# Optimization experiments

Measured on AMD Instinct MI355X. Metric: run time of the kernel, lower is better.

Reference implementation:

```python
import jax, jax.numpy as jnp
import numpy as np


def setup_inputs() -> dict:
    key = jax.random.key(0)
    k1, k2, k3 = jax.random.split(key, 3)
    B, L, d = 4, 9, 256
    n_nodes = (B ** L - 1) // (B - 1)  # complete B-ary tree, level order
    vectors = jax.random.normal(k1, (n_nodes, d), dtype=jnp.float32)
    scale = 1.0 / np.sqrt(d)
    Wl = jax.random.normal(k2, (d, d), dtype=jnp.float32) * scale
    Wr = jax.random.normal(k3, (d, d), dtype=jnp.float32) * scale
    return {"vectors": vectors, "Wl": Wl, "Wr": Wr, "branching": B, "n_levels": L}


def reference(vectors, Wl, Wr, branching, n_levels):
    # Complete branching-ary tree stored in level (BFS) order.
    # Leaf: h = vector. Internal: h = tanh(sum_i lc_i*Wl@h_i + rc_i*Wr@h_i + vector)
    B = int(branching)
    L = int(n_levels)
    sizes = [B ** l for l in range(L)]
    offsets = np.concatenate([[0], np.cumsum(sizes)])
    ind = jnp.arange(1, B + 1, dtype=vectors.dtype)
    if B > 1:
        lc = (B - ind) / (B - 1)   # [B]
        rc = (ind - 1) / (B - 1)
    else:
        lc = jnp.full((B,), 0.5, dtype=vectors.dtype)
        rc = jnp.full((B,), 0.5, dtype=vectors.dtype)
    # leaves
    h = vectors[offsets[L - 1]:offsets[L]]  # [B^(L-1), d]
    for l in range(L - 2, -1, -1):
        n_par = sizes[l]
        hl = (h @ Wl.T).reshape(n_par, B, -1)  # [n_par, B, d]
        hr = (h @ Wr.T).reshape(n_par, B, -1)
        contrib = (lc[None, :, None] * hl + rc[None, :, None] * hr).sum(axis=1)
        h = jnp.tanh(contrib + vectors[offsets[l]:offsets[l + 1]])
    return h  # root state, [1, d]
```

## Files before the change

kernel.cpp:

```cpp
#include <hip/hip_runtime.h>
#include <math.h>


typedef __bf16 bf16x8 __attribute__((ext_vector_type(8)));
typedef __bf16 bf16x4 __attribute__((ext_vector_type(4)));
typedef float f32x4 __attribute__((ext_vector_type(4)));

__device__ __forceinline__ float fast_tanh(float x) {
    float ax = fabsf(x);
    float t = __builtin_amdgcn_exp2f(ax * -2.885390082f);
    float r = (1.0f - t) * __builtin_amdgcn_rcpf(1.0f + t);
    return copysignf(r, x);
}

__global__ __launch_bounds__(256) void cbt_wconv(
    const float* __restrict__ Wl, const float* __restrict__ Wr,
    __bf16* __restrict__ Wfrag)
{
    const int t = blockIdx.x * 256 + threadIdx.x;
    const int L = t & 63;
    const int TJ = t >> 6;
    const int T = TJ & 15;
    const int J = TJ >> 4;
    const int n = J * 16 + (L & 15);
    const int k = T * 32 + (L >> 4) * 8;
    const float* src = (k < 256) ? (Wl + (size_t)n * 256 + k)
                                 : (Wr + (size_t)n * 256 + (k - 256));
    const float4 f0 = *reinterpret_cast<const float4*>(src);
    const float4 f1 = *reinterpret_cast<const float4*>(src + 4);
    bf16x8 o;
    o[0] = (__bf16)f0.x; o[1] = (__bf16)f0.y; o[2] = (__bf16)f0.z; o[3] = (__bf16)f0.w;
    o[4] = (__bf16)f1.x; o[5] = (__bf16)f1.y; o[6] = (__bf16)f1.z; o[7] = (__bf16)f1.w;
    *reinterpret_cast<bf16x8*>(Wfrag + (size_t)t * 8) = o;
}

template <typename CT, typename OT>
__global__ __launch_bounds__(256, 2) void cbt_mfma(
    const CT* __restrict__ h,
    const __bf16* __restrict__ Wfrag,
    const float* __restrict__ vec,
    OT* __restrict__ out)
{
    __shared__ __align__(16) __bf16 Alds[4 * 32 * 40];

    const int tid = threadIdx.x;
    const int lane = tid & 63;
    const int w = tid >> 6;
    const int wr = w >> 1, wc = w & 1;
    const int mBase = blockIdx.x * 32;

    f32x4 acc[8] = {};

    const int sm  = tid >> 3;
    const int skq = (tid & 7) * 4;
    const CT* hb = h + (size_t)(mBase + sm) * 1024 + skq;

    float c0[4], c1[4], c2[4], c3[4];
    auto load_h = [&](int k0) {
        if constexpr (sizeof(CT) == 4) {
            const float4 a = *reinterpret_cast<const float4*>(hb + k0);
            const float4 b = *reinterpret_cast<const float4*>(hb + k0 + 256);
            const float4 c = *reinterpret_cast<const float4*>(hb + k0 + 512);
            const float4 d = *reinterpret_cast<const float4*>(hb + k0 + 768);
            c0[0] = a.x; c0[1] = a.y; c0[2] = a.z; c0[3] = a.w;
            c1[0] = b.x; c1[1] = b.y; c1[2] = b.z; c1[3] = b.w;
            c2[0] = c.x; c2[1] = c.y; c2[2] = c.z; c2[3] = c.w;
            c3[0] = d.x; c3[1] = d.y; c3[2] = d.z; c3[3] = d.w;
        } else {
            const bf16x4 a = *reinterpret_cast<const bf16x4*>(hb + k0);
            const bf16x4 b = *reinterpret_cast<const bf16x4*>(hb + k0 + 256);
            const bf16x4 c = *reinterpret_cast<const bf16x4*>(hb + k0 + 512);
            const bf16x4 d = *reinterpret_cast<const bf16x4*>(hb + k0 + 768);
#pragma unroll
            for (int j = 0; j < 4; ++j) {
                c0[j] = (float)a[j]; c1[j] = (float)b[j];
                c2[j] = (float)c[j]; c3[j] = (float)d[j];
            }
        }
    };

    auto store_A = [&]() {
        constexpr float C23 = 2.0f / 3.0f, C13 = 1.0f / 3.0f;
        bf16x4 glh, gll, grh, grl;
#pragma unroll
        for (int j = 0; j < 4; ++j) {
            const float gl = c0[j] + C23 * c1[j] + C13 * c2[j];
            const float gr = C13 * c1[j] + C23 * c2[j] + c3[j];
            glh[j] = (__bf16)gl;
            gll[j] = (__bf16)(gl - (float)glh[j]);
            grh[j] = (__bf16)gr;
            grl[j] = (__bf16)(gr - (float)grh[j]);
        }
        const int o = sm * 40 + skq;
        *reinterpret_cast<bf16x4*>(&Alds[o])        = glh;
        *reinterpret_cast<bf16x4*>(&Alds[o + 1280]) = gll;
        *reinterpret_cast<bf16x4*>(&Alds[o + 2560]) = grh;
        *reinterpret_cast<bf16x4*>(&Alds[o + 3840]) = grl;
    };

    bf16x8 bfr[2][8];
    const __bf16* Wb = Wfrag + ((size_t)wc * 128 * 64 + lane) * 8;
    auto load_B = [&](int s, int buf) {
        const __bf16* p = Wb + (size_t)s * 512;
#pragma unroll
        for (int j = 0; j < 8; ++j)
            bfr[buf][j] = *reinterpret_cast<const bf16x8*>(p + (size_t)j * 8192);
    };

    load_h(0);
    load_B(0, 0);
    load_B(8, 1);

    const int arow = (wr * 16 + (lane & 15)) * 40 + (lane >> 4) * 8;

    for (int T = 0; T < 8; ++T) {
        __syncthreads();
        store_A();
        __syncthreads();

        if (T < 7) load_h((T + 1) * 32);

        const bf16x8 afLh = *reinterpret_cast<const bf16x8*>(&Alds[arow]);
        const bf16x8 afLl = *reinterpret_cast<const bf16x8*>(&Alds[arow + 1280]);
#pragma unroll
        for (int j = 0; j < 8; ++j)
            acc[j] = __builtin_amdgcn_mfma_f32_16x16x32_bf16(
                afLh, bfr[0][j], acc[j], 0, 0, 0);
#pragma unroll
        for (int j = 0; j < 8; ++j)
            acc[j] = __builtin_amdgcn_mfma_f32_16x16x32_bf16(
                afLl, bfr[0][j], acc[j], 0, 0, 0);

        if (T < 7) load_B(T + 1, 0);

        const bf16x8 afRh = *reinterpret_cast<const bf16x8*>(&Alds[arow + 2560]);
        const bf16x8 afRl = *reinterpret_cast<const bf16x8*>(&Alds[arow + 3840]);
#pragma unroll
        for (int j = 0; j < 8; ++j)
            acc[j] = __builtin_amdgcn_mfma_f32_16x16x32_bf16(
                afRh, bfr[1][j], acc[j], 0, 0, 0);
#pragma unroll
        for (int j = 0; j < 8; ++j)
            acc[j] = __builtin_amdgcn_mfma_f32_16x16x32_bf16(
                afRl, bfr[1][j], acc[j], 0, 0, 0);

        if (T < 7) load_B(T + 9, 1);
    }

    const int q = lane >> 4, n16 = lane & 15;
    const int mrow = mBase + wr * 16 + q * 4;
#pragma unroll
    for (int j = 0; j < 8; ++j) {
        const int n = wc * 128 + j * 16 + n16;
#pragma unroll
        for (int r = 0; r < 4; ++r) {
            const size_t idx = (size_t)(mrow + r) * 256 + n;
            out[idx] = (OT)fast_tanh(acc[j][r] + vec[idx]);
        }
    }
}

__global__ __launch_bounds__(256) void cbt_small(
    const float* __restrict__ h, const float* __restrict__ Wl,
    const float* __restrict__ Wr, const float* __restrict__ vec,
    float* __restrict__ out)
{
    const int w = blockIdx.x * 4 + (threadIdx.x >> 6);
    const int lane = threadIdx.x & 63;
    const int m = w >> 8;
    const int n = w & 255;

    const float* hbp = h + (size_t)m * 1024 + lane * 4;
    const float4 c0 = *reinterpret_cast<const float4*>(hbp);
    const float4 c1 = *reinterpret_cast<const float4*>(hbp + 256);
    const float4 c2 = *reinterpret_cast<const float4*>(hbp + 512);
    const float4 c3 = *reinterpret_cast<const float4*>(hbp + 768);
    const float4 wl = *reinterpret_cast<const float4*>(Wl + (size_t)n * 256 + lane * 4);
    const float4 wr = *reinterpret_cast<const float4*>(Wr + (size_t)n * 256 + lane * 4);

    constexpr float C23 = 2.0f / 3.0f;
    constexpr float C13 = 1.0f / 3.0f;
    const float f0[4] = {c0.x, c0.y, c0.z, c0.w};
    const float f1[4] = {c1.x, c1.y, c1.z, c1.w};
    const float f2[4] = {c2.x, c2.y, c2.z, c2.w};
    const float f3[4] = {c3.x, c3.y, c3.z, c3.w};
    const float wlv[4] = {wl.x, wl.y, wl.z, wl.w};
    const float wrv[4] = {wr.x, wr.y, wr.z, wr.w};
    float acc = 0.0f;
#pragma unroll
    for (int j = 0; j < 4; ++j) {
        const float gl = f0[j] + C23 * f1[j] + C13 * f2[j];
        const float gr = C13 * f1[j] + C23 * f2[j] + f3[j];
        acc += gl * wlv[j] + gr * wrv[j];
    }
#pragma unroll
    for (int off = 32; off >= 1; off >>= 1) acc += __shfl_xor(acc, off, 64);

    if (lane == 0)
        out[(size_t)m * 256 + n] = fast_tanh(acc + vec[(size_t)m * 256 + n]);
}

extern "C" void kernel_launch(void* const* d_in, const int* in_sizes, int n_in,
                              void* d_out, int out_size, void* d_ws, size_t ws_size,
                              hipStream_t stream) {
    const float* vectors = (const float*)d_in[0];
    const float* Wl = (const float*)d_in[1];
    const float* Wr = (const float*)d_in[2];

    char* p = (char*)d_ws;
    __bf16* buf7 = (__bf16*)p;           p += (size_t)16384 * 256 * 2;
    float*  buf6 = (float*)p;            p += (size_t)4096 * 256 * 4;
    float*  buf5 = (float*)p;            p += (size_t)1024 * 256 * 4;
    float*  buf4 = (float*)p;            p += (size_t)256 * 256 * 4;
    float*  buf3 = (float*)p;            p += (size_t)64 * 256 * 4;
    float*  buf2 = (float*)p;            p += (size_t)16 * 256 * 4;
    float*  buf1 = (float*)p;            p += (size_t)4 * 256 * 4;
    __bf16* Wfrag = (__bf16*)p;

    size_t offsets[10];
    offsets[0] = 0;
    size_t sz = 1;
    for (int l = 0; l < 9; ++l) { offsets[l + 1] = offsets[l] + sz; sz *= 4; }

    hipLaunchKernelGGL(cbt_wconv, dim3(64), dim3(256), 0, stream, Wl, Wr, Wfrag);

    const float* leaf = vectors + offsets[8] * 256;

    hipLaunchKernelGGL((cbt_mfma<float, __bf16>), dim3(512), dim3(256), 0, stream,
                       leaf, Wfrag, vectors + offsets[7] * 256, buf7);
    hipLaunchKernelGGL((cbt_mfma<__bf16, float>), dim3(128), dim3(256), 0, stream,
                       buf7, Wfrag, vectors + offsets[6] * 256, buf6);
    hipLaunchKernelGGL((cbt_mfma<float, float>), dim3(32), dim3(256), 0, stream,
                       buf6, Wfrag, vectors + offsets[5] * 256, buf5);
    hipLaunchKernelGGL((cbt_mfma<float, float>), dim3(8), dim3(256), 0, stream,
                       buf5, Wfrag, vectors + offsets[4] * 256, buf4);
    hipLaunchKernelGGL(cbt_small, dim3(64 * 64), dim3(256), 0, stream,
                       buf4, Wl, Wr, vectors + offsets[3] * 256, buf3);
    hipLaunchKernelGGL(cbt_small, dim3(16 * 64), dim3(256), 0, stream,
                       buf3, Wl, Wr, vectors + offsets[2] * 256, buf2);
    hipLaunchKernelGGL(cbt_small, dim3(4 * 64), dim3(256), 0, stream,
                       buf2, Wl, Wr, vectors + offsets[1] * 256, buf1);
    hipLaunchKernelGGL(cbt_small, dim3(1 * 64), dim3(256), 0, stream,
                       buf1, Wl, Wr, vectors + offsets[0] * 256, (float*)d_out);
}
```

Measured before the change: 190.0 us.

## Fuse all tree levels into one cooperative persistent kernel with grid syncs

Replaces the nine separate kernel launches (weight conversion, four MFMA levels, four small levels) with a single cooperative kernel. Grid-wide syncs separate the levels, and grid-stride loops let each block handle several tiles or outputs. The aim is to remove per-launch overhead and inter-kernel gaps, which dominate the tiny upper levels. In exchange it adds grid.sync cost at each level, and the grid is capped at 512 blocks with hardcoded offsets.

```diff
diff --git a/kernel.cpp b/kernel.cpp
--- a/kernel.cpp
+++ b/kernel.cpp
@@ -1,5 +1,8 @@
 #include <hip/hip_runtime.h>
+#include <hip/hip_cooperative_groups.h>
 #include <math.h>
+
+namespace cg = cooperative_groups;
 
 
 typedef __bf16 bf16x8 __attribute__((ext_vector_type(8)));
@@ -13,41 +16,41 @@
     return copysignf(r, x);
 }
 
-__global__ __launch_bounds__(256) void cbt_wconv(
+__device__ __forceinline__ void wconv_body(
     const float* __restrict__ Wl, const float* __restrict__ Wr,
     __bf16* __restrict__ Wfrag)
 {
-    const int t = blockIdx.x * 256 + threadIdx.x;
-    const int L = t & 63;
-    const int TJ = t >> 6;
-    const int T = TJ & 15;
-    const int J = TJ >> 4;
-    const int n = J * 16 + (L & 15);
-    const int k = T * 32 + (L >> 4) * 8;
-    const float* src = (k < 256) ? (Wl + (size_t)n * 256 + k)
-                                 : (Wr + (size_t)n * 256 + (k - 256));
-    const float4 f0 = *reinterpret_cast<const float4*>(src);
-    const float4 f1 = *reinterpret_cast<const float4*>(src + 4);
-    bf16x8 o;
-    o[0] = (__bf16)f0.x; o[1] = (__bf16)f0.y; o[2] = (__bf16)f0.z; o[3] = (__bf16)f0.w;
-    o[4] = (__bf16)f1.x; o[5] = (__bf16)f1.y; o[6] = (__bf16)f1.z; o[7] = (__bf16)f1.w;
-    *reinterpret_cast<bf16x8*>(Wfrag + (size_t)t * 8) = o;
+    for (int t = blockIdx.x * 256 + (int)threadIdx.x; t < 16384;
+         t += gridDim.x * 256) {
+        const int L = t & 63;
+        const int TJ = t >> 6;
+        const int T = TJ & 15;
+        const int J = TJ >> 4;
+        const int n = J * 16 + (L & 15);
+        const int k = T * 32 + (L >> 4) * 8;
+        const float* src = (k < 256) ? (Wl + (size_t)n * 256 + k)
+                                     : (Wr + (size_t)n * 256 + (k - 256));
+        const float4 f0 = *reinterpret_cast<const float4*>(src);
+        const float4 f1 = *reinterpret_cast<const float4*>(src + 4);
+        bf16x8 o;
+        o[0] = (__bf16)f0.x; o[1] = (__bf16)f0.y; o[2] = (__bf16)f0.z; o[3] = (__bf16)f0.w;
+        o[4] = (__bf16)f1.x; o[5] = (__bf16)f1.y; o[6] = (__bf16)f1.z; o[7] = (__bf16)f1.w;
+        *reinterpret_cast<bf16x8*>(Wfrag + (size_t)t * 8) = o;
+    }
 }
 
 template <typename CT, typename OT>
-__global__ __launch_bounds__(256, 2) void cbt_mfma(
+__device__ __forceinline__ void mfma_body(
     const CT* __restrict__ h,
     const __bf16* __restrict__ Wfrag,
     const float* __restrict__ vec,
-    OT* __restrict__ out)
-{
-    __shared__ __align__(16) __bf16 Alds[4 * 32 * 40];
-
+    OT* __restrict__ out,
+    int mBase, __bf16* Alds)
+{
     const int tid = threadIdx.x;
     const int lane = tid & 63;
     const int w = tid >> 6;
     const int wr = w >> 1, wc = w & 1;
-    const int mBase = blockIdx.x * 32;
 
     f32x4 acc[8] = {};
 
@@ -160,44 +163,93 @@
     }
 }
 
-__global__ __launch_bounds__(256) void cbt_small(
+__device__ __forceinline__ void small_body(
     const float* __restrict__ h, const float* __restrict__ Wl,
     const float* __restrict__ Wr, const float* __restrict__ vec,
-    float* __restrict__ out)
-{
-    const int w = blockIdx.x * 4 + (threadIdx.x >> 6);
+    float* __restrict__ out, int nout)
+{
+    const int gw = blockIdx.x * 4 + ((int)threadIdx.x >> 6);
     const int lane = threadIdx.x & 63;
-    const int m = w >> 8;
-    const int n = w & 255;
-
-    const float* hbp = h + (size_t)m * 1024 + lane * 4;
-    const float4 c0 = *reinterpret_cast<const float4*>(hbp);
-    const float4 c1 = *reinterpret_cast<const float4*>(hbp + 256);
-    const float4 c2 = *reinterpret_cast<const float4*>(hbp + 512);
-    const float4 c3 = *reinterpret_cast<const float4*>(hbp + 768);
-    const float4 wl = *reinterpret_cast<const float4*>(Wl + (size_t)n * 256 + lane * 4);
-    const float4 wr = *reinterpret_cast<const float4*>(Wr + (size_t)n * 256 + lane * 4);
-
-    constexpr float C23 = 2.0f / 3.0f;
-    constexpr float C13 = 1.0f / 3.0f;
-    const float f0[4] = {c0.x, c0.y, c0.z, c0.w};
-    const float f1[4] = {c1.x, c1.y, c1.z, c1.w};
-    const float f2[4] = {c2.x, c2.y, c2.z, c2.w};
-    const float f3[4] = {c3.x, c3.y, c3.z, c3.w};
-    const float wlv[4] = {wl.x, wl.y, wl.z, wl.w};
-    const float wrv[4] = {wr.x, wr.y, wr.z, wr.w};
-    float acc = 0.0f;
-#pragma unroll
-    for (int j = 0; j < 4; ++j) {
-        const float gl = f0[j] + C23 * f1[j] + C13 * f2[j];
-        const float gr = C13 * f1[j] + C23 * f2[j] + f3[j];
-        acc += gl * wlv[j] + gr * wrv[j];
-    }
-#pragma unroll
-    for (int off = 32; off >= 1; off >>= 1) acc += __shfl_xor(acc, off, 64);
-
-    if (lane == 0)
-        out[(size_t)m * 256 + n] = fast_tanh(acc + vec[(size_t)m * 256 + n]);
+    const int nw = gridDim.x * 4;
+
+    for (int o = gw; o < nout; o += nw) {
+        const int m = o >> 8;
+        const int n = o & 255;
+
+        const float* hbp = h + (size_t)m * 1024 + lane * 4;
+        const float4 c0 = *reinterpret_cast<const float4*>(hbp);
+        const float4 c1 = *reinterpret_cast<const float4*>(hbp + 256);
+        const float4 c2 = *reinterpret_cast<const float4*>(hbp + 512);
+        const float4 c3 = *reinterpret_cast<const float4*>(hbp + 768);
+        const float4 wl = *reinterpret_cast<const float4*>(Wl + (size_t)n * 256 + lane * 4);
+        const float4 wr = *reinterpret_cast<const float4*>(Wr + (size_t)n * 256 + lane * 4);
+
+        constexpr float C23 = 2.0f / 3.0f;
+        constexpr float C13 = 1.0f / 3.0f;
+        const float f0[4] = {c0.x, c0.y, c0.z, c0.w};
+        const float f1[4] = {c1.x, c1.y, c1.z, c1.w};
+        const float f2[4] = {c2.x, c2.y, c2.z, c2.w};
+        const float f3[4] = {c3.x, c3.y, c3.z, c3.w};
+        const float wlv[4] = {wl.x, wl.y, wl.z, wl.w};
+        const float wrv[4] = {wr.x, wr.y, wr.z, wr.w};
+        float acc = 0.0f;
+#pragma unroll
+        for (int j = 0; j < 4; ++j) {
+            const float gl = f0[j] + C23 * f1[j] + C13 * f2[j];
+            const float gr = C13 * f1[j] + C23 * f2[j] + f3[j];
+            acc += gl * wlv[j] + gr * wrv[j];
+        }
+#pragma unroll
+        for (int off = 32; off >= 1; off >>= 1) acc += __shfl_xor(acc, off, 64);
+
+        if (lane == 0)
+            out[(size_t)m * 256 + n] = fast_tanh(acc + vec[(size_t)m * 256 + n]);
+    }
+}
+
+__global__ __launch_bounds__(256, 2) void cbt_all(
+    const float* __restrict__ vectors,
+    const float* __restrict__ Wl, const float* __restrict__ Wr,
+    float* __restrict__ outF,
+    __bf16* __restrict__ buf7, float* __restrict__ buf6,
+    float* __restrict__ buf5, float* __restrict__ buf4,
+    float* __restrict__ buf3, float* __restrict__ buf2,
+    float* __restrict__ buf1, __bf16* __restrict__ Wfrag)
+{
+    __shared__ __align__(16) __bf16 Alds[4 * 32 * 40];
+
+    cg::grid_group grid = cg::this_grid();
+
+    wconv_body(Wl, Wr, Wfrag);
+    grid.sync();
+
+    for (int t = blockIdx.x; t < 512; t += gridDim.x)
+        mfma_body<float, __bf16>(vectors + (size_t)21845 * 256, Wfrag,
+                                 vectors + (size_t)5461 * 256, buf7, t * 32, Alds);
+    grid.sync();
+
+    for (int t = blockIdx.x; t < 128; t += gridDim.x)
+        mfma_body<__bf16, float>(buf7, Wfrag,
+                                 vectors + (size_t)1365 * 256, buf6, t * 32, Alds);
+    grid.sync();
+
+    for (int t = blockIdx.x; t < 32; t += gridDim.x)
+        mfma_body<float, float>(buf6, Wfrag,
+                                vectors + (size_t)341 * 256, buf5, t * 32, Alds);
+    grid.sync();
+
+    for (int t = blockIdx.x; t < 8; t += gridDim.x)
+        mfma_body<float, float>(buf5, Wfrag,
+                                vectors + (size_t)85 * 256, buf4, t * 32, Alds);
+    grid.sync();
+
+    small_body(buf4, Wl, Wr, vectors + (size_t)21 * 256, buf3, 64 * 256);
+    grid.sync();
+    small_body(buf3, Wl, Wr, vectors + (size_t)5 * 256, buf2, 16 * 256);
+    grid.sync();
+    small_body(buf2, Wl, Wr, vectors + (size_t)1 * 256, buf1, 4 * 256);
+    grid.sync();
+    small_body(buf1, Wl, Wr, vectors, outF, 1 * 256);
 }
 
 extern "C" void kernel_launch(void* const* d_in, const int* in_sizes, int n_in,
@@ -206,6 +258,7 @@
     const float* vectors = (const float*)d_in[0];
     const float* Wl = (const float*)d_in[1];
     const float* Wr = (const float*)d_in[2];
+    float* outF = (float*)d_out;
 
     char* p = (char*)d_ws;
     __bf16* buf7 = (__bf16*)p;           p += (size_t)16384 * 256 * 2;
@@ -217,29 +270,18 @@
     float*  buf1 = (float*)p;            p += (size_t)4 * 256 * 4;
     __bf16* Wfrag = (__bf16*)p;
 
-    size_t offsets[10];
-    offsets[0] = 0;
-    size_t sz = 1;
-    for (int l = 0; l < 9; ++l) { offsets[l + 1] = offsets[l] + sz; sz *= 4; }
-
-    hipLaunchKernelGGL(cbt_wconv, dim3(64), dim3(256), 0, stream, Wl, Wr, Wfrag);
-
-    const float* leaf = vectors + offsets[8] * 256;
-
-    hipLaunchKernelGGL((cbt_mfma<float, __bf16>), dim3(512), dim3(256), 0, stream,
-                       leaf, Wfrag, vectors + offsets[7] * 256, buf7);
-    hipLaunchKernelGGL((cbt_mfma<__bf16, float>), dim3(128), dim3(256), 0, stream,
-                       buf7, Wfrag, vectors + offsets[6] * 256, buf6);
-    hipLaunchKernelGGL((cbt_mfma<float, float>), dim3(32), dim3(256), 0, stream,
-                       buf6, Wfrag, vectors + offsets[5] * 256, buf5);
-    hipLaunchKernelGGL((cbt_mfma<float, float>), dim3(8), dim3(256), 0, stream,
-                       buf5, Wfrag, vectors + offsets[4] * 256, buf4);
-    hipLaunchKernelGGL(cbt_small, dim3(64 * 64), dim3(256), 0, stream,
-                       buf4, Wl, Wr, vectors + offsets[3] * 256, buf3);
-    hipLaunchKernelGGL(cbt_small, dim3(16 * 64), dim3(256), 0, stream,
-                       buf3, Wl, Wr, vectors + offsets[2] * 256, buf2);
-    hipLaunchKernelGGL(cbt_small, dim3(4 * 64), dim3(256), 0, stream,
-                       buf2, Wl, Wr, vectors + offsets[1] * 256, buf1);
-    hipLaunchKernelGGL(cbt_small, dim3(1 * 64), dim3(256), 0, stream,
-                       buf1, Wl, Wr, vectors + offsets[0] * 256, (float*)d_out);
-}
+    int nb = 0;
+    if (hipOccupancyMaxActiveBlocksPerMultiprocessor(&nb, (const void*)cbt_all,
+                                                     256, 0) != hipSuccess || nb < 1)
+        nb = 1;
+    int gridSz = nb * 256;
+    if (gridSz > 512) gridSz = 512;
+
+    void* args[] = {
+        (void*)&vectors, (void*)&Wl, (void*)&Wr, (void*)&outF,
+        (void*)&buf7, (void*)&buf6, (void*)&buf5, (void*)&buf4,
+        (void*)&buf3, (void*)&buf2, (void*)&buf1, (void*)&Wfrag,
+    };
+    hipLaunchCooperativeKernel((const void*)cbt_all, dim3(gridSz), dim3(256),
+                               args, 0, stream);
+}
```

Measured after the change: 429.5 us. +126.0%, slower.

## Fuse tree levels into three launches with software grid barriers

Applied to the files above, without the earlier changes.

The separate weight-conversion kernel is folded into the leaf-level kernel. Extra blocks write Wfrag, while the leaf MFMA path converts Wl/Wr to bf16 on the fly. Levels 5 through 0 now run in one persistent 32-block kernel that uses atomic-counter grid barriers, and the three smallest levels use a shared-memory VALU GEMV split across blocks. This cuts the launch count from nine to three to remove per-launch overhead, at the cost of spin-wait barriers and idle blocks on the small levels.

```diff
diff --git a/kernel.cpp b/kernel.cpp
--- a/kernel.cpp
+++ b/kernel.cpp
@@ -13,41 +13,33 @@
     return copysignf(r, x);
 }
 
-__global__ __launch_bounds__(256) void cbt_wconv(
-    const float* __restrict__ Wl, const float* __restrict__ Wr,
-    __bf16* __restrict__ Wfrag)
-{
-    const int t = blockIdx.x * 256 + threadIdx.x;
-    const int L = t & 63;
-    const int TJ = t >> 6;
-    const int T = TJ & 15;
-    const int J = TJ >> 4;
-    const int n = J * 16 + (L & 15);
-    const int k = T * 32 + (L >> 4) * 8;
-    const float* src = (k < 256) ? (Wl + (size_t)n * 256 + k)
-                                 : (Wr + (size_t)n * 256 + (k - 256));
-    const float4 f0 = *reinterpret_cast<const float4*>(src);
-    const float4 f1 = *reinterpret_cast<const float4*>(src + 4);
-    bf16x8 o;
-    o[0] = (__bf16)f0.x; o[1] = (__bf16)f0.y; o[2] = (__bf16)f0.z; o[3] = (__bf16)f0.w;
-    o[4] = (__bf16)f1.x; o[5] = (__bf16)f1.y; o[6] = (__bf16)f1.z; o[7] = (__bf16)f1.w;
-    *reinterpret_cast<bf16x8*>(Wfrag + (size_t)t * 8) = o;
-}
-
-template <typename CT, typename OT>
-__global__ __launch_bounds__(256, 2) void cbt_mfma(
+__device__ __forceinline__ void kbar(unsigned* cnt, int phase, unsigned nb) {
+    __syncthreads();
+    if (threadIdx.x == 0) {
+        __threadfence();
+        __hip_atomic_fetch_add(&cnt[phase], 1u, __ATOMIC_ACQ_REL,
+                               __HIP_MEMORY_SCOPE_AGENT);
+        while (__hip_atomic_load(&cnt[phase], __ATOMIC_ACQUIRE,
+                                 __HIP_MEMORY_SCOPE_AGENT) < nb)
+            __builtin_amdgcn_s_sleep(1);
+        __threadfence();
+    }
+    __syncthreads();
+}
+
+template <typename CT, typename OT, bool RAWB>
+__device__ __forceinline__ void mfma_body(
     const CT* __restrict__ h,
     const __bf16* __restrict__ Wfrag,
+    const float* __restrict__ Wl, const float* __restrict__ Wr,
     const float* __restrict__ vec,
-    OT* __restrict__ out)
-{
-    __shared__ __align__(16) __bf16 Alds[4 * 32 * 40];
-
+    OT* __restrict__ out,
+    int mBase, __bf16* Alds)
+{
     const int tid = threadIdx.x;
     const int lane = tid & 63;
     const int w = tid >> 6;
     const int wr = w >> 1, wc = w & 1;
-    const int mBase = blockIdx.x * 32;
 
     f32x4 acc[8] = {};
 
@@ -99,12 +91,31 @@
     };
 
     bf16x8 bfr[2][8];
-    const __bf16* Wb = Wfrag + ((size_t)wc * 128 * 64 + lane) * 8;
     auto load_B = [&](int s, int buf) {
-        const __bf16* p = Wb + (size_t)s * 512;
-#pragma unroll
-        for (int j = 0; j < 8; ++j)
-            bfr[buf][j] = *reinterpret_cast<const bf16x8*>(p + (size_t)j * 8192);
+        if constexpr (RAWB) {
+            const int n0 = (wc * 8) * 16 + (lane & 15);
+            const int kk = (s & 7) * 32 + (lane >> 4) * 8;
+            const float* base = (s < 8) ? (Wl + (size_t)n0 * 256 + kk)
+                                        : (Wr + (size_t)n0 * 256 + kk);
+#pragma unroll
+            for (int j = 0; j < 8; ++j) {
+                const float* pp = base + (size_t)j * 4096;
+                const float4 f0 = *reinterpret_cast<const float4*>(pp);
+                const float4 f1 = *reinterpret_cast<const float4*>(pp + 4);
+                bf16x8 o;
+                o[0] = (__bf16)f0.x; o[1] = (__bf16)f0.y;
+                o[2] = (__bf16)f0.z; o[3] = (__bf16)f0.w;
+                o[4] = (__bf16)f1.x; o[5] = (__bf16)f1.y;
+                o[6] = (__bf16)f1.z; o[7] = (__bf16)f1.w;
+                bfr[buf][j] = o;
+            }
+        } else {
+            const __bf16* pq =
+                Wfrag + ((size_t)wc * 8192 + (size_t)s * 64 + lane) * 8;
+#pragma unroll
+            for (int j = 0; j < 8; ++j)
+                bfr[buf][j] = *reinterpret_cast<const bf16x8*>(pq + (size_t)j * 8192);
+        }
     };
 
     load_h(0);
@@ -160,44 +171,131 @@
     }
 }
 
-__global__ __launch_bounds__(256) void cbt_small(
+__global__ __launch_bounds__(256, 2) void cbt_l7(
+    const float* __restrict__ vectors, const float* __restrict__ Wl,
+    const float* __restrict__ Wr, __bf16* __restrict__ buf7,
+    __bf16* __restrict__ Wfrag)
+{
+    __shared__ __align__(16) __bf16 Alds[4 * 32 * 40];
+    if (blockIdx.x >= 512) {
+        const int t = ((int)blockIdx.x - 512) * 256 + (int)threadIdx.x;
+        const int L = t & 63;
+        const int TJ = t >> 6;
+        const int T = TJ & 15;
+        const int J = TJ >> 4;
+        const int n = J * 16 + (L & 15);
+        const int k = T * 32 + (L >> 4) * 8;
+        const float* src = (k < 256) ? (Wl + (size_t)n * 256 + k)
+                                     : (Wr + (size_t)n * 256 + (k - 256));
+        const float4 f0 = *reinterpret_cast<const float4*>(src);
+        const float4 f1 = *reinterpret_cast<const float4*>(src + 4);
+        bf16x8 o;
+        o[0] = (__bf16)f0.x; o[1] = (__bf16)f0.y; o[2] = (__bf16)f0.z; o[3] = (__bf16)f0.w;
+        o[4] = (__bf16)f1.x; o[5] = (__bf16)f1.y; o[6] = (__bf16)f1.z; o[7] = (__bf16)f1.w;
+        *reinterpret_cast<bf16x8*>(Wfrag + (size_t)t * 8) = o;
+        return;
+    }
+    mfma_body<float, __bf16, true>(vectors + (size_t)21845 * 256, nullptr,
+                                   Wl, Wr, vectors + (size_t)5461 * 256,
+                                   buf7, (int)blockIdx.x * 32, Alds);
+}
+
+__global__ __launch_bounds__(256, 2) void cbt_l6(
+    const __bf16* __restrict__ h, const __bf16* __restrict__ Wfrag,
+    const float* __restrict__ vec, float* __restrict__ out,
+    unsigned* __restrict__ bar)
+{
+    if (blockIdx.x == 0 && threadIdx.x < 8) bar[threadIdx.x] = 0;
+    __shared__ __align__(16) __bf16 Alds[4 * 32 * 40];
+    mfma_body<__bf16, float, false>(h, Wfrag, nullptr, nullptr, vec, out,
+                                    (int)blockIdx.x * 32, Alds);
+}
+
+__device__ __forceinline__ void valu_level(
     const float* __restrict__ h, const float* __restrict__ Wl,
     const float* __restrict__ Wr, const float* __restrict__ vec,
-    float* __restrict__ out)
-{
-    const int w = blockIdx.x * 4 + (threadIdx.x >> 6);
-    const int lane = threadIdx.x & 63;
-    const int m = w >> 8;
-    const int n = w & 255;
-
-    const float* hbp = h + (size_t)m * 1024 + lane * 4;
-    const float4 c0 = *reinterpret_cast<const float4*>(hbp);
-    const float4 c1 = *reinterpret_cast<const float4*>(hbp + 256);
-    const float4 c2 = *reinterpret_cast<const float4*>(hbp + 512);
-    const float4 c3 = *reinterpret_cast<const float4*>(hbp + 768);
-    const float4 wl = *reinterpret_cast<const float4*>(Wl + (size_t)n * 256 + lane * 4);
-    const float4 wr = *reinterpret_cast<const float4*>(Wr + (size_t)n * 256 + lane * 4);
-
-    constexpr float C23 = 2.0f / 3.0f;
-    constexpr float C13 = 1.0f / 3.0f;
-    const float f0[4] = {c0.x, c0.y, c0.z, c0.w};
-    const float f1[4] = {c1.x, c1.y, c1.z, c1.w};
-    const float f2[4] = {c2.x, c2.y, c2.z, c2.w};
-    const float f3[4] = {c3.x, c3.y, c3.z, c3.w};
-    const float wlv[4] = {wl.x, wl.y, wl.z, wl.w};
-    const float wrv[4] = {wr.x, wr.y, wr.z, wr.w};
-    float acc = 0.0f;
-#pragma unroll
-    for (int j = 0; j < 4; ++j) {
-        const float gl = f0[j] + C23 * f1[j] + C13 * f2[j];
-        const float gr = C13 * f1[j] + C23 * f2[j] + f3[j];
-        acc += gl * wlv[j] + gr * wrv[j];
-    }
-#pragma unroll
-    for (int off = 32; off >= 1; off >>= 1) acc += __shfl_xor(acc, off, 64);
-
-    if (lane == 0)
-        out[(size_t)m * 256 + n] = fast_tanh(acc + vec[(size_t)m * 256 + n]);
+    float* __restrict__ out, int M, int b, float* G)
+{
+    const int tid = threadIdx.x;
+    constexpr float C23 = 2.0f / 3.0f, C13 = 1.0f / 3.0f;
+    constexpr int GS = 516;
+
+    const int nelem = M * 512;
+    for (int e = tid; e < nelem; e += 256) {
+        const int m = e >> 9, k = e & 511;
+        const float* hm = h + (size_t)m * 1024;
+        float g;
+        if (k < 256)
+            g = hm[k] + C23 * hm[256 + k] + C13 * hm[512 + k];
+        else {
+            const int kk = k - 256;
+            g = C13 * hm[256 + kk] + C23 * hm[512 + kk] + hm[768 + kk];
+        }
+        G[m * GS + k] = g;
+    }
+    __syncthreads();
+
+    const int g16 = tid >> 4, l16 = tid & 15;
+    const int nout = M * 8;
+    for (int o = g16; o < nout; o += 16) {
+        const int m = o >> 3;
+        const int n = b * 8 + (o & 7);
+        const float* wlp = Wl + (size_t)n * 256;
+        const float* wrp = Wr + (size_t)n * 256;
+        float acc = 0.0f;
+#pragma unroll
+        for (int q = 0; q < 8; ++q) {
+            const int k = l16 * 4 + q * 64;
+            const float4 gv = *reinterpret_cast<const float4*>(&G[m * GS + k]);
+            const float4 wv = (q < 4)
+                ? *reinterpret_cast<const float4*>(wlp + k)
+                : *reinterpret_cast<const float4*>(wrp + (k - 256));
+            acc += gv.x * wv.x + gv.y * wv.y + gv.z * wv.z + gv.w * wv.w;
+        }
+#pragma unroll
+        for (int off = 8; off >= 1; off >>= 1)
+            acc += __shfl_xor(acc, off, 64);
+        if (l16 == 0) {
+            const size_t idx = (size_t)m * 256 + n;
+            out[idx] = fast_tanh(acc + vec[idx]);
+        }
+    }
+    __syncthreads();
+}
+
+__global__ __launch_bounds__(256) void cbt_rest(
+    const float* __restrict__ buf6, const __bf16* __restrict__ Wfrag,
+    const float* __restrict__ Wl, const float* __restrict__ Wr,
+    const float* __restrict__ vectors,
+    float* __restrict__ buf5, float* __restrict__ buf4,
+    float* __restrict__ buf3, float* __restrict__ buf2,
+    float* __restrict__ buf1, float* __restrict__ outF,
+    unsigned* __restrict__ bar)
+{
+    __shared__ __align__(16) float shG[16 * 516];
+    __bf16* Alds = (__bf16*)shG;
+    const int b = (int)blockIdx.x;
+    const unsigned NB = 32;
+
+    mfma_body<float, float, false>(buf6, Wfrag, nullptr, nullptr,
+                                   vectors + (size_t)341 * 256, buf5,
+                                   b * 32, Alds);
+    kbar(bar, 0, NB);
+    if (b < 8)
+        mfma_body<float, float, false>(buf5, Wfrag, nullptr, nullptr,
+                                       vectors + (size_t)85 * 256, buf4,
+                                       b * 32, Alds);
+    kbar(bar, 1, NB);
+    if (b < 2)
+        mfma_body<float, float, false>(buf4, Wfrag, nullptr, nullptr,
+                                       vectors + (size_t)21 * 256, buf3,
+                                       b * 32, Alds);
+    kbar(bar, 2, NB);
+    valu_level(buf3, Wl, Wr, vectors + (size_t)5 * 256, buf2, 16, b, shG);
+    kbar(bar, 3, NB);
+    valu_level(buf2, Wl, Wr, vectors + (size_t)1 * 256, buf1, 4, b, shG);
+    kbar(bar, 4, NB);
+    valu_level(buf1, Wl, Wr, vectors, outF, 1, b, shG);
 }
 
 extern "C" void kernel_launch(void* const* d_in, const int* in_sizes, int n_in,
@@ -206,6 +304,7 @@
     const float* vectors = (const float*)d_in[0];
     const float* Wl = (const float*)d_in[1];
     const float* Wr = (const float*)d_in[2];
+    float* outF = (float*)d_out;
 
     char* p = (char*)d_ws;
     __bf16* buf7 = (__bf16*)p;           p += (size_t)16384 * 256 * 2;
@@ -215,31 +314,14 @@
     float*  buf3 = (float*)p;            p += (size_t)64 * 256 * 4;
     float*  buf2 = (float*)p;            p += (size_t)16 * 256 * 4;
     float*  buf1 = (float*)p;            p += (size_t)4 * 256 * 4;
-    __bf16* Wfrag = (__bf16*)p;
-
-    size_t offsets[10];
-    offsets[0] = 0;
-    size_t sz = 1;
-    for (int l = 0; l < 9; ++l) { offsets[l + 1] = offsets[l] + sz; sz *= 4; }
-
-    hipLaunchKernelGGL(cbt_wconv, dim3(64), dim3(256), 0, stream, Wl, Wr, Wfrag);
-
-    const float* leaf = vectors + offsets[8] * 256;
-
-    hipLaunchKernelGGL((cbt_mfma<float, __bf16>), dim3(512), dim3(256), 0, stream,
-                       leaf, Wfrag, vectors + offsets[7] * 256, buf7);
-    hipLaunchKernelGGL((cbt_mfma<__bf16, float>), dim3(128), dim3(256), 0, stream,
-                       buf7, Wfrag, vectors + offsets[6] * 256, buf6);
-    hipLaunchKernelGGL((cbt_mfma<float, float>), dim3(32), dim3(256), 0, stream,
-                       buf6, Wfrag, vectors + offsets[5] * 256, buf5);
-    hipLaunchKernelGGL((cbt_mfma<float, float>), dim3(8), dim3(256), 0, stream,
-                       buf5, Wfrag, vectors + offsets[4] * 256, buf4);
-    hipLaunchKernelGGL(cbt_small, dim3(64 * 64), dim3(256), 0, stream,
-                       buf4, Wl, Wr, vectors + offsets[3] * 256, buf3);
-    hipLaunchKernelGGL(cbt_small, dim3(16 * 64), dim3(256), 0, stream,
-                       buf3, Wl, Wr, vectors + offsets[2] * 256, buf2);
-    hipLaunchKernelGGL(cbt_small, dim3(4 * 64), dim3(256), 0, stream,
-                       buf2, Wl, Wr, vectors + offsets[1] * 256, buf1);
-    hipLaunchKernelGGL(cbt_small, dim3(1 * 64), dim3(256), 0, stream,
-                       buf1, Wl, Wr, vectors + offsets[0] * 256, (float*)d_out);
-}
+    __bf16* Wfrag = (__bf16*)p;          p += (size_t)16384 * 8 * 2;
+    unsigned* bar = (unsigned*)p;
+
+    hipLaunchKernelGGL(cbt_l7, dim3(576), dim3(256), 0, stream,
+                       vectors, Wl, Wr, buf7, Wfrag);
+    hipLaunchKernelGGL(cbt_l6, dim3(128), dim3(256), 0, stream,
+                       buf7, Wfrag, vectors + (size_t)1365 * 256, buf6, bar);
+    hipLaunchKernelGGL(cbt_rest, dim3(32), dim3(256), 0, stream,
+                       buf6, Wfrag, Wl, Wr, vectors,
+                       buf5, buf4, buf3, buf2, buf1, outF, bar);
+}
```

New measurement: 257.7 us. 35.6% more time.
